# Kernel tuning notes

Measured on AMD Instinct MI355X. Metric: run time of the kernel, lower is better.

Reference implementation:

```python
import jax, jax.numpy as jnp
import numpy as np

N_NODES = 50000
N_EDGES = 800000
D_IN = 512
D_HID = 256


def gcn_conv(x, W, b, src, dst, n_nodes):
    """PyG-style GCNConv: self-loops + symmetric normalization.
    x: [N, d_in], W: [d_in, d_out], b: [d_out], src/dst: [E] (already include self-loops? no -> add here)
    """
    loops = jnp.arange(n_nodes, dtype=src.dtype)
    src_f = jnp.concatenate([src, loops])  # [E+N]
    dst_f = jnp.concatenate([dst, loops])
    deg = jax.ops.segment_sum(jnp.ones_like(dst_f, dtype=x.dtype), dst_f,
                              num_segments=n_nodes)  # [N]
    dinv = jnp.where(deg > 0, jax.lax.rsqrt(deg), 0.0)
    norm = dinv[src_f] * dinv[dst_f]  # [E+N]
    h = x @ W  # [N, d_out] -- dense GEMM
    msg = h[src_f] * norm[:, None]  # gather + scale, [E+N, d_out]
    out = jax.ops.segment_sum(msg, dst_f, num_segments=n_nodes)  # scatter-add
    return out + b


def setup_inputs() -> dict:
    key = jax.random.key(0)
    k1, k2, k3, k4, k5 = jax.random.split(key, 5)
    x = jax.random.normal(k1, (N_NODES, D_IN), dtype=jnp.float32)
    edge_index = jax.random.randint(k2, (2, N_EDGES), 0, N_NODES, dtype=jnp.int32)
    # Glorot-ish init for weights
    W1 = jax.random.normal(k3, (D_IN, D_HID), dtype=jnp.float32) / np.sqrt(D_IN)
    W2 = jax.random.normal(k4, (D_HID, D_HID), dtype=jnp.float32) / np.sqrt(D_HID)
    b1 = jnp.zeros((D_HID,), dtype=jnp.float32)
    b2 = jnp.zeros((D_HID,), dtype=jnp.float32)
    return {"x": x, "edge_index": edge_index, "W1": W1, "b1": b1, "W2": W2, "b2": b2}


def reference(x, edge_index, W1, b1, W2, b2):
    n_nodes = x.shape[0]
    src, dst = edge_index[0], edge_index[1]
    h = jax.nn.relu(gcn_conv(x, W1, b1, src, dst, n_nodes))
    h = gcn_conv(h, W2, b2, src, dst, n_nodes)
    # edge-level gather-dot scoring
    score = jnp.einsum('ed,ed->e', h[src], h[dst])  # [E]
    prob_edge = jax.nn.sigmoid(score)
    return prob_edge
```

## Files before the change

### kernel.cpp

```cpp
#include <hip/hip_runtime.h>
#include <stdint.h>

#define D_IN 512
#define D_HID 256

typedef __attribute__((ext_vector_type(8))) short bf16x8;
typedef __attribute__((ext_vector_type(8))) unsigned short u16x8;
typedef __attribute__((ext_vector_type(4))) float f32x4;

__device__ __forceinline__ float b2f(unsigned short u) {
    union { float f; uint32_t i; } x; x.i = ((uint32_t)u) << 16; return x.f;
}
__device__ __forceinline__ unsigned short f2b(float f) {
    union { float f; uint32_t i; } x; x.f = f;
    uint32_t i = x.i;
    uint32_t r = (i + 0x7FFFu + ((i >> 16) & 1u)) >> 16;
    return (unsigned short)r;
}

__device__ __forceinline__ void async_copy16(const unsigned short* g, unsigned short* lds) {
    __builtin_amdgcn_global_load_lds((const __attribute__((address_space(1))) unsigned int*)g,
                                     (__attribute__((address_space(3))) unsigned int*)lds,
                                     16, 0, 0);
}

__global__ __launch_bounds__(256) void detect_dtype_kernel(const ushort4* __restrict__ raw,
                                                           int n4, int* __restrict__ flag) {
    int i = blockIdx.x * blockDim.x + threadIdx.x;
    int hit = 0;
    if (i < n4) {
        ushort4 u = raw[i];
        hit = ((((u.x >> 7) & 0xFF) == 0xFF) || (((u.y >> 7) & 0xFF) == 0xFF) ||
               (((u.z >> 7) & 0xFF) == 0xFF) || (((u.w >> 7) & 0xFF) == 0xFF)) ? 1 : 0;
    }
    unsigned long long b = __ballot(hit);
    if ((threadIdx.x & 63) == 0 && b != 0ULL) atomicOr(flag, 1);
}

__device__ __forceinline__ void wpack_body(const void* __restrict__ W,
        unsigned short* __restrict__ Wp, int K, bool f32, int t) {
    int total = (K >> 6) * 2 * 16 * 64;
    if (t >= total) return;
    int lane = t & 63;
    int c = (t >> 6) & 15;
    int h = (t >> 10) & 1;
    int kk = t >> 11;
    int n = c * 16 + (lane & 15);
    int k0 = kk * 64 + h * 32 + (lane >> 4) * 8;
    u16x8 o;
#pragma unroll
    for (int j = 0; j < 8; ++j) {
        float v = f32 ? ((const float*)W)[(size_t)(k0 + j) * 256 + n]
                      : b2f(((const unsigned short*)W)[(size_t)(k0 + j) * 256 + n]);
        o[j] = f2b(v);
    }
    *(u16x8*)(Wp + (size_t)t * 8) = o;
}

__global__ __launch_bounds__(256) void pre_fused_kernel(const int* __restrict__ dst,
        int* __restrict__ counts, int* __restrict__ within, int E,
        const void* __restrict__ W1, unsigned short* __restrict__ Wp1,
        const void* __restrict__ W2, unsigned short* __restrict__ Wp2,
        const int* __restrict__ flag, int histBlocks, int wp1Blocks) {
    int b = blockIdx.x;
    if (b < histBlocks) {
        int e = b * 256 + threadIdx.x;
        if (e < E) within[e] = atomicAdd(&counts[dst[e]], 1);
        return;
    }
    b -= histBlocks;
    bool f32 = (*flag != 0);
    if (b < wp1Blocks) {
        wpack_body(W1, Wp1, D_IN, f32, b * 256 + threadIdx.x);
    } else {
        wpack_body(W2, Wp2, D_HID, f32, (b - wp1Blocks) * 256 + threadIdx.x);
    }
}

__global__ __launch_bounds__(256) void partial_sum_kernel(const int* __restrict__ counts,
        int* __restrict__ partial, int n) {
    __shared__ int sh[4];
    int b = blockIdx.x;
    int lane = threadIdx.x & 63, wv = threadIdx.x >> 6;
    int s = 0;
    for (int j = threadIdx.x; j < 1024; j += 256) {
        int i = b * 1024 + j;
        s += (i < n) ? counts[i] : 0;
    }
#pragma unroll
    for (int off = 32; off > 0; off >>= 1) s += __shfl_down(s, off, 64);
    if (lane == 0) sh[wv] = s;
    __syncthreads();
    if (threadIdx.x == 0) partial[b] = sh[0] + sh[1] + sh[2] + sh[3];
}

__global__ void scan_partials_kernel(int* __restrict__ partial, int nb,
                                     int* __restrict__ indptr, int N) {
    int lane = threadIdx.x & 63;
    int orig = (lane < nb) ? partial[lane] : 0;
    int v = orig;
#pragma unroll
    for (int off = 1; off < 64; off <<= 1) {
        int u = __shfl(v, lane - off, 64);
        if (lane >= off) v += u;
    }
    int tot = __shfl(v, nb - 1, 64);
    if (lane < nb) partial[lane] = v - orig;
    if (lane == 0) indptr[N] = tot;
}

__global__ __launch_bounds__(1024) void scan_chunk_kernel(const int* __restrict__ counts,
        const int* __restrict__ partial, int* __restrict__ indptr,
        float* __restrict__ dinv, int n) {
    __shared__ int sh[1024];
    int b = blockIdx.x;
    int i = b * 1024 + threadIdx.x;
    int v = (i < n) ? counts[i] : 0;
    sh[threadIdx.x] = v;
    __syncthreads();
    for (int off = 1; off < 1024; off <<= 1) {
        int t = (threadIdx.x >= off) ? sh[threadIdx.x - off] : 0;
        __syncthreads();
        sh[threadIdx.x] += t;
        __syncthreads();
    }
    if (i < n) {
        int e = partial[b] + sh[threadIdx.x] - v;
        indptr[i] = e;
        dinv[i] = rsqrtf((float)(v + 1));
    }
}

template<int K, bool MF32, bool FUSE>
__global__ __launch_bounds__(256) void gemm_bf16(const void* __restrict__ Ain,
        const unsigned short* __restrict__ Wp, unsigned short* __restrict__ C, int M,
        const int* __restrict__ flag,
        const int* __restrict__ eidx, const int* __restrict__ within,
        int* __restrict__ csr_src, int* __restrict__ csr_dst, int* __restrict__ pos_of,
        const int* __restrict__ indptr, int E, int sblocks) {
    __shared__ unsigned short As[2][64 * 64];
    constexpr int NK = K / 64;
    int bid = blockIdx.x;
    int gblocks = (M + 63) >> 6;
    if (FUSE) {
        if (bid >= gblocks) {
            int tb = bid - gblocks;
            if (tb < sblocks) {
                int e = tb * 256 + (int)threadIdx.x;
                if (e < E) {
                    int d = eidx[(size_t)E + e];
                    int pos = indptr[d] + within[e];
                    csr_src[pos] = eidx[e];
                    pos_of[e] = pos;
                }
            } else {
                int v = (tb - sblocks) * 256 + (int)threadIdx.x;
                if (v < M) {
                    int b0 = indptr[v], e0 = indptr[v + 1];
                    for (int p = b0; p < e0; ++p) csr_dst[p] = v;
                }
            }
            return;
        }
    }
    int t = threadIdx.x;
    int lane = t & 63, wv = t >> 6;
    int n0 = lane & 15, grp = lane >> 4;
    int row0 = bid * 64;

    int srow = wv * 16 + (lane >> 3);
    int segp = lane & 7;

    f32x4 acc[4][4];
#pragma unroll
    for (int rt = 0; rt < 4; ++rt)
#pragma unroll
        for (int ct = 0; ct < 4; ++ct) acc[rt][ct] = (f32x4){0.f, 0.f, 0.f, 0.f};

    auto compute_tile = [&](int kk, const unsigned short* Abuf) {
        bf16x8 bw[4][2];
#pragma unroll
        for (int ct = 0; ct < 4; ++ct)
#pragma unroll
            for (int h = 0; h < 2; ++h)
                bw[ct][h] = *(const bf16x8*)(Wp +
                    ((size_t)(((kk * 2 + h) * 16) + (wv * 4 + ct)) * 64 + lane) * 8);
#pragma unroll
        for (int rt = 0; rt < 4; ++rt) {
            int r = rt * 16 + n0;
#pragma unroll
            for (int h = 0; h < 2; ++h) {
                int sp = (h * 4 + grp + r) & 7;
                bf16x8 a = *(const bf16x8*)(Abuf + r * 64 + sp * 8);
#pragma unroll
                for (int ct = 0; ct < 4; ++ct)
                    acc[rt][ct] = __builtin_amdgcn_mfma_f32_16x16x32_bf16(a, bw[ct][h],
                                                                          acc[rt][ct], 0, 0, 0);
            }
        }
    };

    bool f32src = MF32 && (*flag != 0);
    if (f32src) {
        const float* A = (const float*)Ain;
        auto stage_f32 = [&](int buf, const float4* pr) {
#pragma unroll
            for (int j = 0; j < 2; ++j) {
                u16x8 o;
#pragma unroll
                for (int q = 0; q < 4; ++q) {
                    o[q]     = f2b(pr[j * 2 + 0][q]);
                    o[q + 4] = f2b(pr[j * 2 + 1][q]);
                }
                *(u16x8*)(&As[buf][0] + wv * 1024 + j * 512 + lane * 8) = o;
            }
        };
        auto load_f32 = [&](int kof, float4* pr) {
#pragma unroll
            for (int j = 0; j < 2; ++j) {
                int row = srow + j * 8;
                int s = (segp - row) & 7;
                const float* g = A + (size_t)min(row0 + row, M - 1) * K + kof + s * 8;
                pr[j * 2 + 0] = *(const float4*)(g);
                pr[j * 2 + 1] = *(const float4*)(g + 4);
            }
        };
        float4 pr[4];
        load_f32(0, pr);
        stage_f32(0, pr);
        for (int kk = 0; kk < NK; ++kk) {
            int cur = kk & 1;
            if (kk + 1 < NK) load_f32((kk + 1) * 64, pr);
            asm volatile("s_waitcnt lgkmcnt(0)" ::: "memory");
            __builtin_amdgcn_s_barrier();
            compute_tile(kk, &As[cur][0]);
            if (kk + 1 < NK) stage_f32(cur ^ 1, pr);
        }
    } else {
        const unsigned short* A = (const unsigned short*)Ain;
#pragma unroll
        for (int j = 0; j < 2; ++j) {
            int row = srow + j * 8;
            int s = (segp - row) & 7;
            const unsigned short* g = A + (size_t)min(row0 + row, M - 1) * K + s * 8;
            async_copy16(g, &As[0][0] + wv * 1024 + j * 512);
        }
        asm volatile("s_waitcnt vmcnt(0)" ::: "memory");
        __builtin_amdgcn_s_barrier();
        for (int kk = 0; kk < NK; ++kk) {
            int cur = kk & 1;
            if (kk + 1 < NK) {
                int kof = (kk + 1) * 64;
#pragma unroll
                for (int j = 0; j < 2; ++j) {
                    int row = srow + j * 8;
                    int s = (segp - row) & 7;
                    const unsigned short* g = A + (size_t)min(row0 + row, M - 1) * K + kof + s * 8;
                    async_copy16(g, &As[cur ^ 1][0] + wv * 1024 + j * 512);
                }
            }
            compute_tile(kk, &As[cur][0]);
            asm volatile("s_waitcnt vmcnt(0)" ::: "memory");
            __builtin_amdgcn_s_barrier();
        }
    }
#pragma unroll
    for (int rt = 0; rt < 4; ++rt) {
#pragma unroll
        for (int ct = 0; ct < 4; ++ct) {
#pragma unroll
            for (int reg = 0; reg < 4; ++reg) {
                int row = row0 + rt * 16 + grp * 4 + reg;
                if (row < M)
                    C[(size_t)row * 256 + (wv * 4 + ct) * 16 + n0] = f2b(acc[rt][ct][reg]);
            }
        }
    }
}

__global__ __launch_bounds__(256) void aggregate_kernel(const unsigned short* __restrict__ h,
        const int* __restrict__ indptr, const int* __restrict__ csr_src,
        const float* __restrict__ dinv, const void* __restrict__ bias,
        unsigned short* __restrict__ out, int n, int do_relu, const int* __restrict__ flag) {
    int wave = threadIdx.x >> 6;
    int lane = threadIdx.x & 63;
    int half = lane >> 5;
    int hl = lane & 31;
    int v = blockIdx.x * 4 + wave;
    if (v >= n) return;
    int beg = indptr[v];
    int end = indptr[v + 1];
    float dv = dinv[v];

    float acc[8];
    if (half == 0) {
        u16x8 hv = *(const u16x8*)(h + (size_t)v * 256 + hl * 8);
#pragma unroll
        for (int i = 0; i < 8; ++i) acc[i] = dv * b2f(hv[i]);
    } else {
#pragma unroll
        for (int i = 0; i < 8; ++i) acc[i] = 0.f;
    }

    float wA = 0.f, wB = 0.f, wC = 0.f;
    u16x8 rA = (u16x8)0, rB = (u16x8)0, rC = (u16x8)0;
    auto ld = [&](int idx, float& w, u16x8& r) {
        if (idx < end) {
            int s = csr_src[idx];
            w = dinv[s];
            r = *(const u16x8*)(h + (size_t)s * 256 + hl * 8);
        } else {
            w = 0.f;
        }
    };
    int e = beg + half;
    ld(e, wA, rA);
    ld(e + 2, wB, rB);
    ld(e + 4, wC, rC);
    while (e + 4 < end) {
#pragma unroll
        for (int i = 0; i < 8; ++i) acc[i] += wA * b2f(rA[i]);
        ld(e + 6, wA, rA);
#pragma unroll
        for (int i = 0; i < 8; ++i) acc[i] += wB * b2f(rB[i]);
        ld(e + 8, wB, rB);
#pragma unroll
        for (int i = 0; i < 8; ++i) acc[i] += wC * b2f(rC[i]);
        ld(e + 10, wC, rC);
        e += 6;
    }
#pragma unroll
    for (int i = 0; i < 8; ++i)
        acc[i] += wA * b2f(rA[i]) + wB * b2f(rB[i]) + wC * b2f(rC[i]);

#pragma unroll
    for (int i = 0; i < 8; ++i) acc[i] += __shfl_xor(acc[i], 32, 64);

    if (half == 0) {
        float bb[8];
        if (*flag != 0) {
            const float* bp = (const float*)bias + hl * 8;
#pragma unroll
            for (int i = 0; i < 8; ++i) bb[i] = bp[i];
        } else {
            const unsigned short* bp = (const unsigned short*)bias + hl * 8;
#pragma unroll
            for (int i = 0; i < 8; ++i) bb[i] = b2f(bp[i]);
        }
        u16x8 ov;
#pragma unroll
        for (int i = 0; i < 8; ++i) {
            float o = dv * acc[i] + bb[i];
            if (do_relu) o = fmaxf(o, 0.f);
            ov[i] = f2b(o);
        }
        *(u16x8*)(out + (size_t)v * 256 + hl * 8) = ov;
    }
}

__global__ __launch_bounds__(256) void edge_score_mfma(const unsigned short* __restrict__ h,
        const int* __restrict__ csr_src, const int* __restrict__ csr_dst,
        float* __restrict__ tmp, int E) {
    int lane = threadIdx.x & 63;
    int wv = threadIdx.x >> 6;
    int base = (blockIdx.x * 4 + wv) * 16;
    if (base >= E) return;
    int m = lane & 15, grp = lane >> 4;
    int e = base + m;
    int ec = min(e, E - 1);
    int s = csr_src[ec], d = csr_dst[ec];
    const unsigned short* hs = h + (size_t)s * 256 + grp * 8;
    const unsigned short* hd = h + (size_t)d * 256 + grp * 8;
    f32x4 acc = {0.f, 0.f, 0.f, 0.f};
#pragma unroll
    for (int kk = 0; kk < 8; ++kk) {
        bf16x8 a = *(const bf16x8*)(hs + kk * 32);
        bf16x8 b = *(const bf16x8*)(hd + kk * 32);
        acc = __builtin_amdgcn_mfma_f32_16x16x32_bf16(a, b, acc, 0, 0, 0);
    }
    int reg = m - grp * 4;
    if (reg >= 0 && reg < 4 && e < E) {
        float p = (reg == 0) ? acc[0] : (reg == 1) ? acc[1] : (reg == 2) ? acc[2] : acc[3];
        tmp[e] = 1.f / (1.f + __expf(-p));
    }
}

__global__ __launch_bounds__(256) void permute_out_kernel(const float* __restrict__ tmp,
        const int* __restrict__ pos_of, void* __restrict__ out, int E,
        const int* __restrict__ flag) {
    int e = blockIdx.x * blockDim.x + threadIdx.x;
    if (e >= E) return;
    float p = tmp[pos_of[e]];
    if (*flag != 0)
        ((float*)out)[e] = p;
    else
        ((unsigned short*)out)[e] = f2b(p);
}

extern "C" void kernel_launch(void* const* d_in, const int* in_sizes, int n_in,
                              void* d_out, int out_size, void* d_ws, size_t ws_size,
                              hipStream_t stream) {
    const void* x  = d_in[0];
    const int* edge_index = (const int*)d_in[1];
    const void* W1 = d_in[2];
    const void* b1 = d_in[3];
    const void* W2 = d_in[4];
    const void* b2 = d_in[5];

    const int N = in_sizes[0] / D_IN;
    const int E = in_sizes[1] / 2;
    const int* dst = edge_index + E;

    char* ws = (char*)d_ws;
    size_t off = 0;
    auto alloc = [&](size_t bytes) {
        char* p = ws + off;
        off = (off + bytes + 255) & ~(size_t)255;
        return p;
    };
    int* flag     = (int*)alloc(256);
    float* dinv   = (float*)alloc((size_t)N * 4);
    int* counts   = (int*)alloc((size_t)N * 4);
    int* indptr   = (int*)alloc((size_t)(N + 1) * 4);
    int* partial  = (int*)alloc(64 * 4);
    int* within   = (int*)alloc((size_t)E * 4);
    int* csr_src  = (int*)alloc((size_t)E * 4);
    int* csr_dst  = (int*)alloc((size_t)E * 4);
    int* pos_of   = (int*)alloc((size_t)E * 4);
    float* ptmp   = (float*)alloc((size_t)E * 4);
    unsigned short* Wp1 = (unsigned short*)alloc((size_t)D_IN * 256 * 2);
    unsigned short* Wp2 = (unsigned short*)alloc((size_t)D_HID * 256 * 2);
    unsigned short* hA  = (unsigned short*)alloc((size_t)N * 256 * 2);
    unsigned short* hB  = (unsigned short*)alloc((size_t)N * 256 * 2);

    const int nb = (N + 1023) / 1024;
    const int sblocks = (E + 255) / 256;
    const int fblocks = (N + 255) / 256;
    const int wp1Blocks = (D_IN * 32) / 256;
    const int wp2Blocks = (D_HID * 32) / 256;
    const int ggrid = (N + 63) / 64;

    hipMemsetAsync(flag, 0, 4, stream);
    hipMemsetAsync(counts, 0, (size_t)N * 4, stream);
    detect_dtype_kernel<<<64, 256, 0, stream>>>((const ushort4*)x, 16384, flag);
    pre_fused_kernel<<<sblocks + wp1Blocks + wp2Blocks, 256, 0, stream>>>(
        dst, counts, within, E, W1, Wp1, W2, Wp2, flag, sblocks, wp1Blocks);
    partial_sum_kernel<<<nb, 256, 0, stream>>>(counts, partial, N);
    scan_partials_kernel<<<1, 64, 0, stream>>>(partial, nb, indptr, N);
    scan_chunk_kernel<<<nb, 1024, 0, stream>>>(counts, partial, indptr, dinv, N);

    gemm_bf16<D_IN, true, true><<<ggrid + sblocks + fblocks, 256, 0, stream>>>(
        x, Wp1, hA, N, flag, edge_index, within, csr_src, csr_dst, pos_of, indptr, E, sblocks);
    aggregate_kernel<<<(N + 3) / 4, 256, 0, stream>>>(hA, indptr, csr_src, dinv, b1, hB, N, 1, flag);
    gemm_bf16<D_HID, false, false><<<ggrid, 256, 0, stream>>>(
        hB, Wp2, hA, N, flag, nullptr, nullptr, nullptr, nullptr, nullptr, nullptr, 0, 0);
    aggregate_kernel<<<(N + 3) / 4, 256, 0, stream>>>(hA, indptr, csr_src, dinv, b2, hB, N, 0, flag);
    edge_score_mfma<<<(E + 63) / 64, 256, 0, stream>>>(hB, csr_src, csr_dst, ptmp, E);
    permute_out_kernel<<<(E + 255) / 256, 256, 0, stream>>>(ptmp, pos_of, d_out, E, flag);
}
```

Baseline: 444.3 us.

## Fold counts memset into detect kernel, double edges per thread, preload full K=256 tile

Three changes. The memset of the degree counts is folded into extra blocks of the dtype-detect kernel, which removes one stream operation. Each histogram thread now handles two edges so that two atomics are in flight per thread. The K=256 GEMM issues async loads for all four K slices into LDS up front and then computes them without intermediate barriers. This trades more LDS per block (32KB), which may lower occupancy, for fewer synchronisation points.

```diff
diff --git a/kernel.cpp b/kernel.cpp
--- a/kernel.cpp
+++ b/kernel.cpp
@@ -25,16 +25,22 @@
 }
 
 __global__ __launch_bounds__(256) void detect_dtype_kernel(const ushort4* __restrict__ raw,
-                                                           int n4, int* __restrict__ flag) {
-    int i = blockIdx.x * blockDim.x + threadIdx.x;
+        int n4, int* __restrict__ flag, int* __restrict__ counts, int N, int dblocks) {
+    int b = blockIdx.x;
+    if (b >= dblocks) {
+        int i = (b - dblocks) * 256 + threadIdx.x;
+        if (i < N) counts[i] = 0;
+        return;
+    }
+    int i = b * 256 + threadIdx.x;
     int hit = 0;
     if (i < n4) {
         ushort4 u = raw[i];
         hit = ((((u.x >> 7) & 0xFF) == 0xFF) || (((u.y >> 7) & 0xFF) == 0xFF) ||
                (((u.z >> 7) & 0xFF) == 0xFF) || (((u.w >> 7) & 0xFF) == 0xFF)) ? 1 : 0;
     }
-    unsigned long long b = __ballot(hit);
-    if ((threadIdx.x & 63) == 0 && b != 0ULL) atomicOr(flag, 1);
+    unsigned long long bl = __ballot(hit);
+    if ((threadIdx.x & 63) == 0 && bl != 0ULL) atomicOr(flag, 1);
 }
 
 __device__ __forceinline__ void wpack_body(const void* __restrict__ W,
@@ -64,8 +70,19 @@
         const int* __restrict__ flag, int histBlocks, int wp1Blocks) {
     int b = blockIdx.x;
     if (b < histBlocks) {
+        int halfE = (E + 1) >> 1;
         int e = b * 256 + threadIdx.x;
-        if (e < E) within[e] = atomicAdd(&counts[dst[e]], 1);
+        if (e < halfE) {
+            int d1 = dst[e];
+            int e2 = e + halfE;
+            if (e2 < E) {
+                int d2 = dst[e2];
+                within[e]  = atomicAdd(&counts[d1], 1);
+                within[e2] = atomicAdd(&counts[d2], 1);
+            } else {
+                within[e] = atomicAdd(&counts[d1], 1);
+            }
+        }
         return;
     }
     b -= histBlocks;
@@ -138,7 +155,7 @@
         const int* __restrict__ eidx, const int* __restrict__ within,
         int* __restrict__ csr_src, int* __restrict__ csr_dst, int* __restrict__ pos_of,
         const int* __restrict__ indptr, int E, int sblocks) {
-    __shared__ unsigned short As[2][64 * 64];
+    __shared__ unsigned short As[(K == 256) ? 4 : 2][64 * 64];
     constexpr int NK = K / 64;
     int bid = blockIdx.x;
     int gblocks = (M + 63) >> 6;
@@ -236,6 +253,23 @@
             compute_tile(kk, &As[cur][0]);
             if (kk + 1 < NK) stage_f32(cur ^ 1, pr);
         }
+    } else if constexpr (K == 256) {
+        const unsigned short* A = (const unsigned short*)Ain;
+#pragma unroll
+        for (int kk = 0; kk < 4; ++kk) {
+#pragma unroll
+            for (int j = 0; j < 2; ++j) {
+                int row = srow + j * 8;
+                int s = (segp - row) & 7;
+                const unsigned short* g = A + (size_t)min(row0 + row, M - 1) * K
+                                           + kk * 64 + s * 8;
+                async_copy16(g, &As[kk][0] + wv * 1024 + j * 512);
+            }
+        }
+        asm volatile("s_waitcnt vmcnt(0)" ::: "memory");
+        __builtin_amdgcn_s_barrier();
+#pragma unroll
+        for (int kk = 0; kk < 4; ++kk) compute_tile(kk, &As[kk][0]);
     } else {
         const unsigned short* A = (const unsigned short*)Ain;
 #pragma unroll
@@ -434,17 +468,20 @@
     unsigned short* hB  = (unsigned short*)alloc((size_t)N * 256 * 2);
 
     const int nb = (N + 1023) / 1024;
+    const int halfE = (E + 1) / 2;
+    const int histBlocks = (halfE + 255) / 256;
     const int sblocks = (E + 255) / 256;
     const int fblocks = (N + 255) / 256;
     const int wp1Blocks = (D_IN * 32) / 256;
     const int wp2Blocks = (D_HID * 32) / 256;
     const int ggrid = (N + 63) / 64;
+    const int dblocks = 64;
 
     hipMemsetAsync(flag, 0, 4, stream);
-    hipMemsetAsync(counts, 0, (size_t)N * 4, stream);
-    detect_dtype_kernel<<<64, 256, 0, stream>>>((const ushort4*)x, 16384, flag);
-    pre_fused_kernel<<<sblocks + wp1Blocks + wp2Blocks, 256, 0, stream>>>(
-        dst, counts, within, E, W1, Wp1, W2, Wp2, flag, sblocks, wp1Blocks);
+    detect_dtype_kernel<<<dblocks + fblocks, 256, 0, stream>>>(
+        (const ushort4*)x, 16384, flag, counts, N, dblocks);
+    pre_fused_kernel<<<histBlocks + wp1Blocks + wp2Blocks, 256, 0, stream>>>(
+        dst, counts, within, E, W1, Wp1, W2, Wp2, flag, histBlocks, wp1Blocks);
     partial_sum_kernel<<<nb, 256, 0, stream>>>(counts, partial, N);
     scan_partials_kernel<<<1, 64, 0, stream>>>(partial, nb, indptr, N);
     scan_chunk_kernel<<<nb, 1024, 0, stream>>>(counts, partial, indptr, dinv, N);
```

Result: no change. 443.5 us (-0.2%).
